# Kernel tuning notes

Hardware: AMD Instinct MI355X
Metric: run time of the kernel (lower is better)

## Reference

```python
import jax, jax.numpy as jnp
import numpy as np

N = 100000      # nodes
E = 1600000     # directed edges (before self loops)
F_IN = 3        # node_feature_dim
H = 32          # hidden_dim
BN_EPS = 1e-5


def _linear_params(k, fan_in, fan_out):
    lim = 1.0 / np.sqrt(fan_in)
    kw, kb = jax.random.split(k)
    W = jax.random.uniform(kw, (fan_in, fan_out), jnp.float32, -lim, lim)
    b = jax.random.uniform(kb, (fan_out,), jnp.float32, -lim, lim)
    return W, b


def setup_inputs() -> dict:
    key = jax.random.key(0)
    ks = jax.random.split(key, 12)
    x = jax.random.normal(ks[0], (N, F_IN), jnp.float32)
    edge_index = jax.random.randint(ks[1], (2, E), 0, N, dtype=jnp.int64)
    node_type = jax.random.randint(ks[2], (N,), 0, 3, dtype=jnp.int64)
    W1, b1 = _linear_params(ks[3], F_IN, H)
    W2, b2 = _linear_params(ks[4], H, H)
    W3, b3 = _linear_params(ks[5], H, H)
    g1 = jnp.ones((H,), jnp.float32); be1 = jnp.zeros((H,), jnp.float32)
    g2 = jnp.ones((H,), jnp.float32); be2 = jnp.zeros((H,), jnp.float32)
    Wc1, bc1 = _linear_params(ks[6], H, H // 2)
    Wc2, bc2 = _linear_params(ks[7], H // 2, 1)
    Wd1, bd1 = _linear_params(ks[8], H, H // 2)
    Wd2, bd2 = _linear_params(ks[9], H // 2, 1)
    return dict(x=x, edge_index=edge_index, node_type=node_type,
                W1=W1, b1=b1, W2=W2, b2=b2, W3=W3, b3=b3,
                g1=g1, be1=be1, g2=g2, be2=be2,
                Wc1=Wc1, bc1=bc1, Wc2=Wc2, bc2=bc2,
                Wd1=Wd1, bd1=bd1, Wd2=Wd2, bd2=bd2)


def reference(x, edge_index, node_type, W1, b1, W2, b2, W3, b3,
              g1, be1, g2, be2, Wc1, bc1, Wc2, bc2, Wd1, bd1, Wd2, bd2):
    n = x.shape[0]
    # GCNConv (PyG default): add self loops, symmetric deg^-1/2 normalization
    loop = jnp.arange(n, dtype=edge_index.dtype)
    src = jnp.concatenate([edge_index[0], loop])  # [E+N]
    dst = jnp.concatenate([edge_index[1], loop])
    deg = jax.ops.segment_sum(jnp.ones_like(dst, dtype=x.dtype), dst, num_segments=n)
    dinv = jnp.where(deg > 0, jax.lax.rsqrt(jnp.maximum(deg, 1.0)), 0.0)
    norm = dinv[src] * dinv[dst]  # [E+N]

    def conv(h, W, b):
        msg = (h @ W)[src] * norm[:, None]                  # gather + scale
        return jax.ops.segment_sum(msg, dst, num_segments=n) + b  # scatter-add

    def bn(h, g, be):  # BatchNorm1d with batch statistics (training math)
        mu = h.mean(axis=0)
        var = ((h - mu) ** 2).mean(axis=0)
        return (h - mu) * jax.lax.rsqrt(var + BN_EPS) * g + be

    h = bn(jax.nn.relu(conv(x, W1, b1)), g1, be1)   # dropout = identity (eval)
    h = bn(jax.nn.relu(conv(h, W2, b2)), g2, be2)
    h = jax.nn.relu(conv(h, W3, b3))

    cand_mask = node_type == 0
    cand_emb = h[cand_mask]                                 # [C, H]
    cand_scores = (jax.nn.relu(cand_emb @ Wc1 + bc1) @ Wc2 + bc2)[:, 0]

    w = jax.nn.softmax(h.sum(axis=1))[:, None]              # [N,1] importance
    g_emb = (h * w).sum(axis=0, keepdims=True)              # [1, H]
    dn = (jax.nn.relu(g_emb @ Wd1 + bd1) @ Wd2 + bd2).reshape(())

    logits = jnp.concatenate([cand_scores, dn[None]], axis=0)
    cand_idx = jnp.nonzero(cand_mask)[0]
    return logits, cand_idx
```

## Files before the change

kernel.cpp:

```cpp
#include <hip/hip_runtime.h>

typedef unsigned int uint;
typedef unsigned char uchar;

#define NB_MAX 256
#define NPB_MAX 2048

#if defined(__has_builtin)
#if __has_builtin(__builtin_amdgcn_cvt_pk_f32_fp8) && __has_builtin(__builtin_amdgcn_cvt_pk_fp8_f32)
#define HW_FP8 1
#endif
#endif

typedef __attribute__((ext_vector_type(2))) float v2f;

static __device__ __forceinline__ uint f2fp8_sw(float v) {
    v = fminf(fmaxf(v, -448.f), 448.f);
    uint u = __float_as_uint(v);
    uint s = (u >> 24) & 0x80u;
    uint mag = u & 0x7FFFFFFFu;
    uint r = mag + 0x7FFFFu + ((mag >> 20) & 1u);
    if (r < 0x3C800000u) return s;
    uint e8 = (r - 0x3C000000u) >> 20;
    return s | min(e8, 0x7Eu);
}
static __device__ __forceinline__ float fp82f(uint b) {
    uint mag = b & 0x7Fu;
    uint bits = ((b & 0x80u) << 24) | ((mag << 20) + 0x3C000000u);
    return mag ? __uint_as_float(bits) : 0.f;
}
static __device__ __forceinline__ void dec8(uint2 v, float* o) {
#ifdef HW_FP8
    v2f a = __builtin_amdgcn_cvt_pk_f32_fp8((int)v.x, false);
    v2f b = __builtin_amdgcn_cvt_pk_f32_fp8((int)v.x, true);
    v2f c = __builtin_amdgcn_cvt_pk_f32_fp8((int)v.y, false);
    v2f d = __builtin_amdgcn_cvt_pk_f32_fp8((int)v.y, true);
    o[0]=a.x; o[1]=a.y; o[2]=b.x; o[3]=b.y;
    o[4]=c.x; o[5]=c.y; o[6]=d.x; o[7]=d.y;
#else
// ... 29 lines not shown
}

static __device__ __forceinline__ unsigned wave_incl_scan(unsigned v) {
    int lane = threadIdx.x & 63;
    #pragma unroll
    for (int d = 1; d < 64; d <<= 1) {
        unsigned t = (unsigned)__shfl_up((int)v, d, 64);
        if (lane >= d) v += t;
    }
    return v;
}

static __device__ void block_excl_scan(const uint* in, uint* out, int n, uint* wscr) {
    int tid = threadIdx.x;
    int lane = tid & 63, wid = tid >> 6;
    int base = tid * 8;
    uint v[8], pre[8], s = 0;
    #pragma unroll
    for (int k = 0; k < 8; k++) v[k] = (base + k < n) ? in[base + k] : 0u;
    #pragma unroll
    for (int k = 0; k < 8; k++) { pre[k] = s; s += v[k]; }
    uint is = wave_incl_scan(s);
    __syncthreads();
    if (lane == 63) wscr[wid] = is;
    __syncthreads();
    uint woff = 0;
    for (int wI = 0; wI < wid; wI++) woff += wscr[wI];
    uint excl = is - s + woff;
    #pragma unroll
    for (int k = 0; k < 8; k++) if (base + k < n) out[base + k] = excl + pre[k];
    __syncthreads();
}

__global__ __launch_bounds__(256) void bucket_hist_kernel(const int* src, const int* dst,
                                                          const int* nt, uint* bcnt, uint* bcand,
                                                          int E, int N, int NB, int shift) {
    __shared__ uint bh[NB_MAX], ch[NB_MAX];
    int tid = threadIdx.x;
    bh[tid] = 0; ch[tid] = 0;
    __syncthreads();
    int gs = gridDim.x * 256;
    for (int i = blockIdx.x * 256 + tid; i < E; i += gs) {
        int d = dst[i], s = src[i];
        if ((uint)d < (uint)N && (uint)s < (uint)N) atomicAdd(&bh[d >> shift], 1u);
    }
    for (int i = blockIdx.x * 256 + tid; i < N; i += gs) {
        if (nt[i] == 0) atomicAdd(&ch[i >> shift], 1u);
    }
    __syncthreads();
    if (bh[tid]) atomicAdd(&bcnt[tid], bh[tid]);
    if (ch[tid]) atomicAdd(&bcand[tid], ch[tid]);
}

__global__ __launch_bounds__(256) void partition_kernel(const int* src, const int* dst,
                                                        const uint* bcnt, uint* alloc0,
                                                        uint* staging, int E, int N, int shift) {
    __shared__ uint bbase_s[NB_MAX];
    __shared__ uint lh[NB_MAX], gb[NB_MAX];
    __shared__ uint ws4[4];
    int tid = threadIdx.x;
    int lane = tid & 63, wid = tid >> 6;
    uint a = bcnt[tid];
    uint ia = wave_incl_scan(a);
    if (lane == 63) ws4[wid] = ia;
    __syncthreads();
    uint off = 0;
    for (int wI = 0; wI < wid; wI++) off += ws4[wI];
    bbase_s[tid] = ia - a + off;
    lh[tid] = 0;
    __syncthreads();
    int base = blockIdx.x * 2048;
    uint mask = (1u << shift) - 1u;
    int breg[8];
    uint rreg[8], pk8[8];
    #pragma unroll
    for (int k = 0; k < 8; k++) {
        int e = base + k * 256 + tid;
        breg[k] = -1;
        if (e < E) {
            int s = src[e], d = dst[e];
            if ((uint)d < (uint)N && (uint)s < (uint)N) {
                int b = d >> shift;
                pk8[k] = (((uint)d & mask) << 17) | (uint)s;
                breg[k] = b;
                rreg[k] = atomicAdd(&lh[b], 1u);
            }
        }
    }
    __syncthreads();
    gb[tid] = lh[tid] ? (bbase_s[tid] + atomicAdd(&alloc0[tid], lh[tid])) : 0u;
    __syncthreads();
    #pragma unroll
    for (int k = 0; k < 8; k++) {
        if (breg[k] >= 0)
            staging[gb[breg[k]] + rreg[k]] = pk8[k];
    }
}

__global__ __launch_bounds__(256) void local_csr_kernel(const uint* staging, const uint* bcnt,
                                                        const uint* bcand, const int* nt,
                                                        const float* x,
                                                        int* csr_src, uint* csr_off, uint* cand_pos,
                                                        float* dinv, float4* xs,
                                                        int N, int shift, int NB) {
    __shared__ uint deg[NPB_MAX];
    __shared__ uint ofs[NPB_MAX];
    __shared__ uint ws4[4];
    __shared__ uint sb[4];
    int b = blockIdx.x, tid = threadIdx.x;
    int lane = tid & 63, wid = tid >> 6;
    uint a = bcnt[tid];
    uint ia = wave_incl_scan(a);
    if (lane == 63) ws4[wid] = ia;
    __syncthreads();
    uint off = 0;
    for (int wI = 0; wI < wid; wI++) off += ws4[wI];
    if (tid == b) { sb[0] = ia - a + off; sb[1] = ia + off; }
    __syncthreads();
    uint c = bcand[tid];
    uint ic = wave_incl_scan(c);
    if (lane == 63) ws4[wid] = ic;
    __syncthreads();
    uint offc = 0;
    for (int wI = 0; wI < wid; wI++) offc += ws4[wI];
    if (tid == b) sb[2] = ic - c + offc;
    __syncthreads();
    uint ebase = sb[0], eend = sb[1], cb = sb[2];
    int nbase = b << shift;
    int ncount = min(1 << shift, N - nbase);
    for (int i = tid; i < ncount; i += 256) deg[i] = 0;
    __syncthreads();
    for (uint p = ebase + tid; p < eend; p += 256)
        atomicAdd(&deg[staging[p] >> 17], 1u);
    __syncthreads();
    block_excl_scan(deg, ofs, ncount, ws4);
    for (int i = tid; i < ncount; i += 256)
        csr_off[nbase + i] = ebase + ofs[i];
    if (b == NB - 1 && tid == 0) csr_off[N] = eend;
    for (int i = tid; i < ncount; i += 256) {
        int g = nbase + i;
        float di = rsqrtf((float)(deg[i] + 1u));
        dinv[g] = di;
        xs[g] = make_float4(x[3*g] * di, x[3*g+1] * di, x[3*g+2] * di, 0.f);
    }
    __syncthreads();
    for (int i = tid; i < ncount; i += 256) deg[i] = 0;
    __syncthreads();
    for (uint p = ebase + tid; p < eend; p += 256) {
        uint pkv = staging[p];
        uint dl = pkv >> 17;
        uint pos = ebase + ofs[dl] + atomicAdd(&deg[dl], 1u);
        csr_src[pos] = (int)(pkv & 0x1FFFFu);
    }
    __syncthreads();
    for (int i = tid; i < ncount; i += 256) deg[i] = (nt[nbase + i] == 0) ? 1u : 0u;
    __syncthreads();
    block_excl_scan(deg, ofs, ncount, ws4);
    for (int i = tid; i < ncount; i += 256) cand_pos[nbase + i] = cb + ofs[i];
}

__global__ __launch_bounds__(256) void agg1_kernel(const float* xs, const int* csr_src,
                                                   const uint* csr_off, const float* dinv,
                                                   const float* W1, const float* b1, uchar* hb,
                                                   int n, float* stats_sum, float* stats_sq,
                                                   uint* gt) {
    const int tid = threadIdx.x;
    const int wave = tid >> 6;
    const int lane = tid & 63;
    const int c4 = lane & 3;
    const int slot = lane >> 2;
    const int qlead = lane & ~3;
    __shared__ float W1s[96];
    __shared__ uint s_lt, s_chunk;
    if (tid < 96) W1s[tid] = W1[tid];
    float bv[8];
    #pragma unroll
    for (int j = 0; j < 8; j++) bv[j] = b1[c4 * 8 + j];
    float bs[8], bq[8];
    #pragma unroll
    for (int j = 0; j < 8; j++) { bs[j] = 0.f; bq[j] = 0.f; }
    __syncthreads();
    while (true) {
        if (tid == 0) s_chunk = atomicAdd(gt, 1u);
        __syncthreads();
        uint cbase = s_chunk * 128u;
        if (cbase >= (uint)n) break;
        uint avail = min((uint)n - cbase, 128u);
        if (tid == 0) s_lt = 0u;
        __syncthreads();
        while (true) {
            uint li = 0;
            if (c4 == 0) li = atomicAdd(&s_lt, 1u);
            li = (uint)__shfl((int)li, qlead, 64);
            if (li >= avail) break;
            uint node = cbase + li;
            uint s = csr_off[node], e = csr_off[node + 1];
            float acc = xs[(size_t)node * 4 + c4];
            for (uint p = s; p < e; p += 8) {
                uint idx[8];
                float wg[8];
                #pragma unroll
                for (int j = 0; j < 8; j++) {
                    uint q = p + (uint)j;
                    uint qc = min(q, e - 1u);
                    idx[j] = (uint)csr_src[qc];
                    wg[j] = (q < e) ? 1.f : 0.f;
                }
                #pragma unroll
                for (int j = 0; j < 8; j++)
                    acc = fmaf(wg[j], xs[(size_t)idx[j] * 4 + c4], acc);
            }
            float u = dinv[node] * acc;
            float u0 = __shfl(u, qlead, 64);
            float u1 = __shfl(u, qlead + 1, 64);
            float u2 = __shfl(u, qlead + 2, 64);
            float hv[8];
            #pragma unroll
            for (int j = 0; j < 8; j++) {
                int ch = c4 * 8 + j;
                float o = u0 * W1s[ch] + u1 * W1s[32 + ch] + u2 * W1s[64 + ch] + bv[j];
                hv[j] = fmaxf(o, 0.f);
            }
            *(uint2*)(hb + (size_t)node * 32 + c4 * 8) = enc8(hv);
            #pragma unroll
            for (int j = 0; j < 8; j++) { bs[j] += hv[j]; bq[j] += hv[j] * hv[j]; }
        }
        __syncthreads();
    }
    #pragma unroll
    for (int m = 4; m < 64; m <<= 1) {
        #pragma unroll
        for (int j = 0; j < 8; j++) {
            bs[j] += __shfl_xor(bs[j], m, 64);
            bq[j] += __shfl_xor(bq[j], m, 64);
        }
    }
    __shared__ float ssum[4][32], ssq[4][32];
    if (slot == 0) {
        #pragma unroll
        for (int j = 0; j < 8; j++) { ssum[wave][c4 * 8 + j] = bs[j]; ssq[wave][c4 * 8 + j] = bq[j]; }
    }
    __syncthreads();
    if (tid < 32) {
        atomicAdd(&stats_sum[tid], ssum[0][tid] + ssum[1][tid] + ssum[2][tid] + ssum[3][tid]);
        atomicAdd(&stats_sq[tid],  ssq[0][tid] + ssq[1][tid] + ssq[2][tid] + ssq[3][tid]);
    }
}

__global__ __launch_bounds__(256) void gemmf_kernel(const uchar* hb, const float* stats_sum,
                                                    const float* stats_sq, const float* g,
                                                    const float* be, const float* W,
                                                    const float* dinv, uchar* zb, int n,
                                                    float inv_n) {
    __shared__ float Ws[1024];
    __shared__ float cs[32];
    __shared__ float a_s[32], d_s[32];
    int tid = threadIdx.x;
    if (tid < 32) {
        float mu = stats_sum[tid] * inv_n;
        float var = fmaxf(stats_sq[tid] * inv_n - mu * mu, 0.f);
        float a = g[tid] * rsqrtf(var + 1e-5f);
        a_s[tid] = a;
        d_s[tid] = be[tid] - mu * a;
    }
    __syncthreads();
    #pragma unroll
    for (int t = tid; t < 1024; t += 256) Ws[t] = a_s[t >> 5] * W[t];
    if (tid < 32) {
        float c = 0.f;
        for (int k = 0; k < 32; k++) c += d_s[k] * W[k * 32 + tid];
        cs[tid] = c;
    }
    __syncthreads();
    int i = blockIdx.x * 256 + tid;
    if (i >= n) return;
    float hk[32], acc[32];
    dec32(hb + (size_t)i * 32, hk);
    #pragma unroll
    for (int j = 0; j < 32; j++) acc[j] = cs[j];
    #pragma unroll
    for (int k = 0; k < 32; k++) {
        float h0 = hk[k];
        #pragma unroll
        for (int j = 0; j < 32; j++) acc[j] += h0 * Ws[k * 32 + j];
    }
    float di = dinv[i];
    #pragma unroll
    for (int j = 0; j < 32; j++) acc[j] *= di;
    enc32(acc, zb + (size_t)i * 32);
}

template<int MODE>
__global__ __launch_bounds__(256) void agg_kernel(const uchar* zb, const int* csr_src,
                                                  const uint* csr_off, const float* dinv,
                                                  const float* bias, uchar* hb, int n,
                                                  float* stats_sum, float* stats_sq,
                                                  float* rowsum, uint* maxkey, uint* gt) {
    const int tid = threadIdx.x;
    const int wave = tid >> 6;
    const int lane = tid & 63;
    const int c4 = lane & 3;
    const int slot = lane >> 2;
    const int qlead = lane & ~3;
    __shared__ uint s_lt, s_chunk;
    float bv[8];
    #pragma unroll
    for (int j = 0; j < 8; j++) bv[j] = bias[c4 * 8 + j];
    float bs[8], bq[8];
    if (MODE == 0) {
        #pragma unroll
        for (int j = 0; j < 8; j++) { bs[j] = 0.f; bq[j] = 0.f; }
    }
    float lmax = -3.0e38f;
    while (true) {
        if (tid == 0) s_chunk = atomicAdd(gt, 1u);
        __syncthreads();
        uint cbase = s_chunk * 128u;
        if (cbase >= (uint)n) break;
        uint avail = min((uint)n - cbase, 128u);
        if (tid == 0) s_lt = 0u;
        __syncthreads();
        while (true) {
            uint li = 0;
            if (c4 == 0) li = atomicAdd(&s_lt, 1u);
            li = (uint)__shfl((int)li, qlead, 64);
            if (li >= avail) break;
            uint node = cbase + li;
            uint s = csr_off[node], e = csr_off[node + 1];
            float acc[8];
            dec8(*(const uint2*)(zb + (size_t)node * 32 + c4 * 8), acc);
            for (uint p = s; p < e; p += 8) {
                uint idx[8];
                float wg[8];
                #pragma unroll
                for (int j = 0; j < 8; j++) {
                    uint q = p + (uint)j;
                    uint qc = min(q, e - 1u);
                    idx[j] = (uint)csr_src[qc];
                    wg[j] = (q < e) ? 1.f : 0.f;
                }
                #pragma unroll
                for (int j = 0; j < 8; j++) {
                    float t[8];
                    dec8(*(const uint2*)(zb + (size_t)idx[j] * 32 + c4 * 8), t);
                    #pragma unroll
                    for (int cI = 0; cI < 8; cI++) acc[cI] = fmaf(wg[j], t[cI], acc[cI]);
                }
            }
            float di = dinv[node];
            float hv[8];
            #pragma unroll
            for (int j = 0; j < 8; j++) hv[j] = fmaxf(di * acc[j] + bv[j], 0.f);
            *(uint2*)(hb + (size_t)node * 32 + c4 * 8) = enc8(hv);
            if (MODE == 0) {
                #pragma unroll
                for (int j = 0; j < 8; j++) { bs[j] += hv[j]; bq[j] += hv[j] * hv[j]; }
            } else {
                float rs = ((hv[0] + hv[1]) + (hv[2] + hv[3])) + ((hv[4] + hv[5]) + (hv[6] + hv[7]));
                rs += __shfl_xor(rs, 1, 64);
                rs += __shfl_xor(rs, 2, 64);
                if (c4 == 0) { rowsum[node] = rs; lmax = fmaxf(lmax, rs); }
            }
        }
        __syncthreads();
    }
    if (MODE == 0) {
        #pragma unroll
        for (int m = 4; m < 64; m <<= 1) {
            #pragma unroll
            for (int j = 0; j < 8; j++) {
                bs[j] += __shfl_xor(bs[j], m, 64);
                bq[j] += __shfl_xor(bq[j], m, 64);
            }
        }
        __shared__ float ssum[4][32], ssq[4][32];
        if (slot == 0) {
            #pragma unroll
            for (int j = 0; j < 8; j++) { ssum[wave][c4 * 8 + j] = bs[j]; ssq[wave][c4 * 8 + j] = bq[j]; }
        }
        __syncthreads();
        if (tid < 32) {
            atomicAdd(&stats_sum[tid], ssum[0][tid] + ssum[1][tid] + ssum[2][tid] + ssum[3][tid]);
            atomicAdd(&stats_sq[tid],  ssq[0][tid] + ssq[1][tid] + ssq[2][tid] + ssq[3][tid]);
        }
    } else {
        #pragma unroll
        for (int m = 1; m < 64; m <<= 1) lmax = fmaxf(lmax, __shfl_xor(lmax, m, 64));
        __shared__ float lm[4];
        if (lane == 0) lm[wave] = lmax;
        __syncthreads();
        if (tid == 0) {
            float m = fmaxf(fmaxf(lm[0], lm[1]), fmaxf(lm[2], lm[3]));
            uint u = __float_as_uint(m);
            uint key = (u & 0x80000000u) ? ~u : (u | 0x80000000u);
            atomicMax(maxkey, key);
        }
    }
}

__global__ __launch_bounds__(256) void head_kernel(const uchar* hb, const int* nt,
                                                   const uint* pos, const float* Wc1,
                                                   const float* bc1, const float* Wc2,
                                                   const float* bc2, const float* rowsum,
                                                   const uint* maxkey, float* gvec, float* Zp,
                                                   uint* ticket, const float* Wd1,
                                                   const float* bd1, const float* Wd2,
                                                   const float* bd2, float* out, int n, int C) {
    __shared__ float W1s[512], b1s[16], W2s[16];
    __shared__ float ls[256];
    __shared__ float ge[32], tt[16];
    __shared__ int lastflag;
    int tid = threadIdx.x;
    for (int t = tid; t < 512; t += 256) W1s[t] = Wc1[t];
    if (tid < 16) { b1s[tid] = bc1[tid]; W2s[tid] = Wc2[tid]; }
    __syncthreads();
    int i = blockIdx.x * 256 + tid;
    if (i < n && nt[i] == 0) {
        float hv[32];
        dec32(hb + (size_t)i * 32, hv);
        float s = bc2[0];
        #pragma unroll
        for (int j = 0; j < 16; j++) {
            float u = b1s[j];
            #pragma unroll
            for (int k = 0; k < 32; k++) u += hv[k] * W1s[k * 16 + j];
            s += fmaxf(u, 0.f) * W2s[j];
        }
        s = fminf(fmaxf(s, -1000.f), 1000.f);
        uint p = pos[i];
        if (p < (uint)C) {
            out[p] = s;
            out[C + 1 + p] = (float)i;
        }
    }
    uint key = *maxkey;
    float M = 0.f;
    if (key != 0u) M = (key & 0x80000000u) ? __uint_as_float(key ^ 0x80000000u) : __uint_as_float(~key);
    int lane = tid & 31, grp = tid >> 5;
    int stride = gridDim.x * 8;
    float accZ = 0.f, accg = 0.f;
    for (int node = blockIdx.x * 8 + grp; node < n; node += stride) {
        float ew = __expf(rowsum[node] - M);
        accg += fp82f(hb[(size_t)node * 32 + lane]) * ew;
        if (lane == 0) accZ += ew;
    }
    ls[tid] = accg;
    __syncthreads();
    if (tid < 32) {
        float a = 0.f;
        #pragma unroll
        for (int g = 0; g < 8; g++) a += ls[tid + 32 * g];
        atomicAdd(&gvec[tid], a);
    }
    __syncthreads();
    ls[tid] = (lane == 0) ? accZ : 0.f;
    __syncthreads();
    if (tid == 0) {
        float a = 0.f;
        for (int t = 0; t < 256; t += 32) a += ls[t];
        atomicAdd(Zp, a);
        __threadfence();
        uint old = atomicAdd(ticket, 1u);
        lastflag = (old == gridDim.x - 1) ? 1 : 0;
    }
    __syncthreads();
    if (lastflag) {
        __threadfence();
        if (tid < 32) ge[tid] = atomicAdd(&gvec[tid], 0.f);
        if (tid == 0) ls[0] = atomicAdd(Zp, 0.f);
        __syncthreads();
        float Zv = fmaxf(ls[0], 1e-30f);
        if (tid < 32) ge[tid] /= Zv;
        __syncthreads();
        if (tid < 16) {
            float s = bd1[tid];
            for (int k = 0; k < 32; k++) s += ge[k] * Wd1[k * 16 + tid];
            tt[tid] = fmaxf(s, 0.f);
        }
        __syncthreads();
        if (tid == 0) {
            float s = bd2[0];
            for (int j = 0; j < 16; j++) s += tt[j] * Wd2[j];
            out[C] = fminf(fmaxf(s, -1000.f), 1000.f);
        }
    }
}

extern "C" void kernel_launch(void* const* d_in, const int* in_sizes, int n_in,
                              void* d_out, int out_size, void* d_ws, size_t ws_size,
                              hipStream_t stream) {
    const float* x   = (const float*)d_in[0];
    const int*   ei  = (const int*)d_in[1];
    const int*   nt  = (const int*)d_in[2];
    const float* W1  = (const float*)d_in[3];  const float* b1  = (const float*)d_in[4];
    const float* W2  = (const float*)d_in[5];  const float* b2  = (const float*)d_in[6];
    const float* W3  = (const float*)d_in[7];  const float* b3  = (const float*)d_in[8];
    const float* g1  = (const float*)d_in[9];  const float* be1 = (const float*)d_in[10];
    const float* g2  = (const float*)d_in[11]; const float* be2 = (const float*)d_in[12];
    const float* Wc1 = (const float*)d_in[13]; const float* bc1 = (const float*)d_in[14];
    const float* Wc2 = (const float*)d_in[15]; const float* bc2 = (const float*)d_in[16];
    const float* Wd1 = (const float*)d_in[17]; const float* bd1 = (const float*)d_in[18];
    const float* Wd2 = (const float*)d_in[19]; const float* bd2 = (const float*)d_in[20];

    const int N = in_sizes[0] / 3;
    const int E = in_sizes[1] / 2;
    const int C = (out_size - 1) / 2;
    const int* e_src = ei;
    const int* e_dst = ei + E;
    float* out = (float*)d_out;

    int shift = 9;
    while (((N + (1 << shift) - 1) >> shift) > NB_MAX) shift++;
    const int NB = (N + (1 << shift) - 1) >> shift;

    char* w = (char*)d_ws;
    auto alloc = [&](size_t bytes) { void* p = (void*)w; w += (bytes + 255) & ~(size_t)255; return p; };
    float*    stats  = (float*)alloc(256 * 4);
    uint*     bcnt   = (uint*)alloc(NB_MAX * 4);
    uint*     bcand  = (uint*)alloc(NB_MAX * 4);
    uint*     alloc0 = (uint*)alloc(NB_MAX * 4);
    size_t zero_bytes = (size_t)((char*)w - (char*)stats);
    float*    dinv   = (float*)alloc((size_t)N * 4);
    uint*     csr_off= (uint*)alloc((size_t)(N + 1) * 4);
    uint*     cand_pos=(uint*)alloc((size_t)N * 4);
    float*    rowsum = (float*)alloc((size_t)N * 4);
    int*      csr_src= (int*)alloc((size_t)E * 4);
    uint*     staging= (uint*)alloc((size_t)E * 4);
    uchar*    zb     = (uchar*)alloc((size_t)N * 32);
    uchar*    hb     = (uchar*)alloc((size_t)N * 32);
    float4*   xs     = (float4*)zb;

    float* sum1 = stats;       float* sq1 = stats + 32;
    float* sum2 = stats + 64;  float* sq2 = stats + 96;
    float* gvec = stats + 128; float* Zp  = stats + 160;
    uint* maxkey = (uint*)(stats + 161);
    uint* ticket = (uint*)(stats + 162);
    uint* gt1 = (uint*)(stats + 163);
    uint* gt2 = (uint*)(stats + 164);
    uint* gt3 = (uint*)(stats + 165);

    hipMemsetAsync(stats, 0, zero_bytes, stream);

    const int gN   = (N + 255) / 256;
    const int gPar = (E + 2047) / 2048;
    int gAgg = (N + 127) / 128;
    if (gAgg > 512) gAgg = 512;
    const float inv_n = 1.0f / (float)N;

    hipLaunchKernelGGL(bucket_hist_kernel, dim3(784), dim3(256), 0, stream, e_src, e_dst, nt, bcnt, bcand, E, N, NB, shift);
    hipLaunchKernelGGL(partition_kernel, dim3(gPar), dim3(256), 0, stream, e_src, e_dst, bcnt, alloc0, staging, E, N, shift);
    hipLaunchKernelGGL(local_csr_kernel, dim3(NB), dim3(256), 0, stream, staging, bcnt, bcand, nt,
                       x, csr_src, csr_off, cand_pos, dinv, xs, N, shift, NB);

    hipLaunchKernelGGL(agg1_kernel, dim3(gAgg), dim3(256), 0, stream, (const float*)xs, csr_src, csr_off,
                       dinv, W1, b1, hb, N, sum1, sq1, gt1);

    hipLaunchKernelGGL(gemmf_kernel, dim3(gN), dim3(256), 0, stream, hb, sum1, sq1, g1, be1, W2, dinv, zb, N, inv_n);
    hipLaunchKernelGGL((agg_kernel<0>), dim3(gAgg), dim3(256), 0, stream, zb, csr_src, csr_off,
                       dinv, b2, hb, N, sum2, sq2, rowsum, maxkey, gt2);

    hipLaunchKernelGGL(gemmf_kernel, dim3(gN), dim3(256), 0, stream, hb, sum2, sq2, g2, be2, W3, dinv, zb, N, inv_n);
    hipLaunchKernelGGL((agg_kernel<1>), dim3(gAgg), dim3(256), 0, stream, zb, csr_src, csr_off,
                       dinv, b3, hb, N, sum1, sq1, rowsum, maxkey, gt3);

    hipLaunchKernelGGL(head_kernel, dim3(gN), dim3(256), 0, stream, hb, nt, cand_pos,
                       Wc1, bc1, Wc2, bc2, rowsum, maxkey, gvec, Zp, ticket,
                       Wd1, bd1, Wd2, bd2, out, N, C);
}
```

Before: 318.1 us.

## Fuse all stages into one persistent kernel with software grid barriers

Replaces the nine separate kernel launches with a single persistent mega-kernel of fixed grid size. Each former kernel becomes a device phase with grid-stride loops, and the phases are separated by atomic-counter grid barriers. Shared memory is merged through a union. This aims to remove launch gaps and per-kernel tail drain. It relies on all 448 blocks being co-resident, otherwise the barriers deadlock, and the fixed grid may underfill or overfill phases that previously had their own grid sizes.

```diff
diff --git a/kernel.cpp b/kernel.cpp
--- a/kernel.cpp
+++ b/kernel.cpp
@@ -5,6 +5,7 @@
 
 #define NB_MAX 256
 #define NPB_MAX 2048
+#define GRID_BLKS 448
 
 #if defined(__has_builtin)
 #if __has_builtin(__builtin_amdgcn_cvt_pk_f32_fp8) && __has_builtin(__builtin_amdgcn_cvt_pk_fp8_f32)
@@ -100,185 +101,211 @@
     __syncthreads();
 }
 
-__global__ __launch_bounds__(256) void bucket_hist_kernel(const int* src, const int* dst,
-                                                          const int* nt, uint* bcnt, uint* bcand,
-                                                          int E, int N, int NB, int shift) {
-    __shared__ uint bh[NB_MAX], ch[NB_MAX];
+union ShU {
+    struct { uint bh[NB_MAX]; uint ch[NB_MAX]; } hist;
+    struct { uint bbase[NB_MAX]; uint lh[NB_MAX]; uint gb[NB_MAX]; uint ws4[4]; } part;
+    struct { uint deg[NPB_MAX]; uint ofs[NPB_MAX]; uint ws4[4]; uint sb[4]; } csr;
+    struct { float Ws[1024]; float cs[32]; float a_s[32]; float d_s[32]; } gemm;
+    struct { float W1s[96]; float ssum[4][32]; float ssq[4][32]; float lm[4]; uint s_lt; uint s_chunk; } agg;
+    struct { float W1s[512]; float b1s[16]; float W2s[16]; float ls[256]; float ge[32]; float tt[16]; } head;
+};
+
+struct MegaP {
+    const float* x;
+    const int* e_src; const int* e_dst; const int* nt;
+    const float *W1,*b1,*W2,*b2,*W3,*b3;
+    const float *g1,*be1,*g2,*be2;
+    const float *Wc1,*bc1,*Wc2,*bc2,*Wd1,*bd1,*Wd2,*bd2;
+    float* stats;
+    uint *bcnt,*bcand,*alloc0;
+    float* dinv; uint* csr_off; uint* cand_pos; float* rowsum;
+    int* csr_src; uint* staging;
+    uchar *zb,*hb;
+    float* out;
+    int N,E,C,NB,shift,nPar;
+    float inv_n;
+};
+
+static __device__ __forceinline__ void gbar(uint* ctr, uint nblk) {
+    __syncthreads();
+    if (threadIdx.x == 0) {
+        __threadfence();
+        uint v = atomicAdd(ctr, 1u) + 1u;
+        while (v < nblk) {
+            __builtin_amdgcn_s_sleep(8);
+            v = __hip_atomic_load(ctr, __ATOMIC_RELAXED, __HIP_MEMORY_SCOPE_AGENT);
+        }
+        __threadfence();
+    }
+    __syncthreads();
+}
+
+static __device__ __forceinline__ void ph_hist(const MegaP& p, ShU& sh) {
     int tid = threadIdx.x;
-    bh[tid] = 0; ch[tid] = 0;
+    sh.hist.bh[tid] = 0; sh.hist.ch[tid] = 0;
     __syncthreads();
     int gs = gridDim.x * 256;
-    for (int i = blockIdx.x * 256 + tid; i < E; i += gs) {
-        int d = dst[i], s = src[i];
-        if ((uint)d < (uint)N && (uint)s < (uint)N) atomicAdd(&bh[d >> shift], 1u);
-    }
-    for (int i = blockIdx.x * 256 + tid; i < N; i += gs) {
-        if (nt[i] == 0) atomicAdd(&ch[i >> shift], 1u);
-    }
-    __syncthreads();
-    if (bh[tid]) atomicAdd(&bcnt[tid], bh[tid]);
-    if (ch[tid]) atomicAdd(&bcand[tid], ch[tid]);
-}
-
-__global__ __launch_bounds__(256) void partition_kernel(const int* src, const int* dst,
-                                                        const uint* bcnt, uint* alloc0,
-                                                        uint* staging, int E, int N, int shift) {
-    __shared__ uint bbase_s[NB_MAX];
-    __shared__ uint lh[NB_MAX], gb[NB_MAX];
-    __shared__ uint ws4[4];
+    for (int i = blockIdx.x * 256 + tid; i < p.E; i += gs) {
+        int d = p.e_dst[i], s = p.e_src[i];
+        if ((uint)d < (uint)p.N && (uint)s < (uint)p.N) atomicAdd(&sh.hist.bh[d >> p.shift], 1u);
+    }
+    for (int i = blockIdx.x * 256 + tid; i < p.N; i += gs) {
+        if (p.nt[i] == 0) atomicAdd(&sh.hist.ch[i >> p.shift], 1u);
+    }
+    __syncthreads();
+    if (sh.hist.bh[tid]) atomicAdd(&p.bcnt[tid], sh.hist.bh[tid]);
+    if (sh.hist.ch[tid]) atomicAdd(&p.bcand[tid], sh.hist.ch[tid]);
+}
+
+static __device__ __forceinline__ void ph_partition(const MegaP& p, ShU& sh) {
     int tid = threadIdx.x;
     int lane = tid & 63, wid = tid >> 6;
-    uint a = bcnt[tid];
+    uint a = p.bcnt[tid];
     uint ia = wave_incl_scan(a);
-    if (lane == 63) ws4[wid] = ia;
+    if (lane == 63) sh.part.ws4[wid] = ia;
     __syncthreads();
     uint off = 0;
-    for (int wI = 0; wI < wid; wI++) off += ws4[wI];
-    bbase_s[tid] = ia - a + off;
-    lh[tid] = 0;
-    __syncthreads();
-    int base = blockIdx.x * 2048;
-    uint mask = (1u << shift) - 1u;
-    int breg[8];
-    uint rreg[8], pk8[8];
-    #pragma unroll
-    for (int k = 0; k < 8; k++) {
-        int e = base + k * 256 + tid;
-        breg[k] = -1;
-        if (e < E) {
-            int s = src[e], d = dst[e];
-            if ((uint)d < (uint)N && (uint)s < (uint)N) {
-                int b = d >> shift;
-                pk8[k] = (((uint)d & mask) << 17) | (uint)s;
-                breg[k] = b;
-                rreg[k] = atomicAdd(&lh[b], 1u);
-            }
-        }
-    }
-    __syncthreads();
-    gb[tid] = lh[tid] ? (bbase_s[tid] + atomicAdd(&alloc0[tid], lh[tid])) : 0u;
-    __syncthreads();
-    #pragma unroll
-    for (int k = 0; k < 8; k++) {
-        if (breg[k] >= 0)
-            staging[gb[breg[k]] + rreg[k]] = pk8[k];
-    }
-}
-
-__global__ __launch_bounds__(256) void local_csr_kernel(const uint* staging, const uint* bcnt,
-                                                        const uint* bcand, const int* nt,
-                                                        const float* x,
-                                                        int* csr_src, uint* csr_off, uint* cand_pos,
-                                                        float* dinv, float4* xs,
-                                                        int N, int shift, int NB) {
-    __shared__ uint deg[NPB_MAX];
-    __shared__ uint ofs[NPB_MAX];
-    __shared__ uint ws4[4];
-    __shared__ uint sb[4];
-    int b = blockIdx.x, tid = threadIdx.x;
+    for (int wI = 0; wI < wid; wI++) off += sh.part.ws4[wI];
+    sh.part.bbase[tid] = ia - a + off;
+    __syncthreads();
+    uint mask = (1u << p.shift) - 1u;
+    for (int cb = blockIdx.x; cb < p.nPar; cb += gridDim.x) {
+        sh.part.lh[tid] = 0;
+        __syncthreads();
+        int base = cb * 2048;
+        int breg[8];
+        uint rreg[8], pk8[8];
+        #pragma unroll
+        for (int k = 0; k < 8; k++) {
+            int e = base + k * 256 + tid;
+            breg[k] = -1;
+            if (e < p.E) {
+                int s = p.e_src[e], d = p.e_dst[e];
+                if ((uint)d < (uint)p.N && (uint)s < (uint)p.N) {
+                    int b = d >> p.shift;
+                    pk8[k] = (((uint)d & mask) << 17) | (uint)s;
+                    breg[k] = b;
+                    rreg[k] = atomicAdd(&sh.part.lh[b], 1u);
+                }
+            }
+        }
+        __syncthreads();
+        sh.part.gb[tid] = sh.part.lh[tid] ? (sh.part.bbase[tid] + atomicAdd(&p.alloc0[tid], sh.part.lh[tid])) : 0u;
+        __syncthreads();
+        #pragma unroll
+        for (int k = 0; k < 8; k++) {
+            if (breg[k] >= 0)
+                p.staging[sh.part.gb[breg[k]] + rreg[k]] = pk8[k];
+        }
+        __syncthreads();
+    }
+}
+
+static __device__ __forceinline__ void ph_localcsr(const MegaP& p, ShU& sh) {
+    int tid = threadIdx.x;
     int lane = tid & 63, wid = tid >> 6;
-    uint a = bcnt[tid];
-    uint ia = wave_incl_scan(a);
-    if (lane == 63) ws4[wid] = ia;
-    __syncthreads();
-    uint off = 0;
-    for (int wI = 0; wI < wid; wI++) off += ws4[wI];
-    if (tid == b) { sb[0] = ia - a + off; sb[1] = ia + off; }
-    __syncthreads();
-    uint c = bcand[tid];
-    uint ic = wave_incl_scan(c);
-    if (lane == 63) ws4[wid] = ic;
-    __syncthreads();
-    uint offc = 0;
-    for (int wI = 0; wI < wid; wI++) offc += ws4[wI];
-    if (tid == b) sb[2] = ic - c + offc;
-    __syncthreads();
-    uint ebase = sb[0], eend = sb[1], cb = sb[2];
-    int nbase = b << shift;
-    int ncount = min(1 << shift, N - nbase);
-    for (int i = tid; i < ncount; i += 256) deg[i] = 0;
-    __syncthreads();
-    for (uint p = ebase + tid; p < eend; p += 256)
-        atomicAdd(&deg[staging[p] >> 17], 1u);
-    __syncthreads();
-    block_excl_scan(deg, ofs, ncount, ws4);
-    for (int i = tid; i < ncount; i += 256)
-        csr_off[nbase + i] = ebase + ofs[i];
-    if (b == NB - 1 && tid == 0) csr_off[N] = eend;
-    for (int i = tid; i < ncount; i += 256) {
-        int g = nbase + i;
-        float di = rsqrtf((float)(deg[i] + 1u));
-        dinv[g] = di;
-        xs[g] = make_float4(x[3*g] * di, x[3*g+1] * di, x[3*g+2] * di, 0.f);
-    }
-    __syncthreads();
-    for (int i = tid; i < ncount; i += 256) deg[i] = 0;
-    __syncthreads();
-    for (uint p = ebase + tid; p < eend; p += 256) {
-        uint pkv = staging[p];
-        uint dl = pkv >> 17;
-        uint pos = ebase + ofs[dl] + atomicAdd(&deg[dl], 1u);
-        csr_src[pos] = (int)(pkv & 0x1FFFFu);
-    }
-    __syncthreads();
-    for (int i = tid; i < ncount; i += 256) deg[i] = (nt[nbase + i] == 0) ? 1u : 0u;
-    __syncthreads();
-    block_excl_scan(deg, ofs, ncount, ws4);
-    for (int i = tid; i < ncount; i += 256) cand_pos[nbase + i] = cb + ofs[i];
-}
-
-__global__ __launch_bounds__(256) void agg1_kernel(const float* xs, const int* csr_src,
-                                                   const uint* csr_off, const float* dinv,
-                                                   const float* W1, const float* b1, uchar* hb,
-                                                   int n, float* stats_sum, float* stats_sq,
-                                                   uint* gt) {
+    float4* xs = (float4*)p.zb;
+    for (int b = blockIdx.x; b < p.NB; b += gridDim.x) {
+        uint a = p.bcnt[tid];
+        uint ia = wave_incl_scan(a);
+        if (lane == 63) sh.csr.ws4[wid] = ia;
+        __syncthreads();
+        uint off = 0;
+        for (int wI = 0; wI < wid; wI++) off += sh.csr.ws4[wI];
+        if (tid == b) { sh.csr.sb[0] = ia - a + off; sh.csr.sb[1] = ia + off; }
+        __syncthreads();
+        uint c = p.bcand[tid];
+        uint ic = wave_incl_scan(c);
+        if (lane == 63) sh.csr.ws4[wid] = ic;
+        __syncthreads();
+        uint offc = 0;
+        for (int wI = 0; wI < wid; wI++) offc += sh.csr.ws4[wI];
+        if (tid == b) sh.csr.sb[2] = ic - c + offc;
+        __syncthreads();
+        uint ebase = sh.csr.sb[0], eend = sh.csr.sb[1], cbv = sh.csr.sb[2];
+        int nbase = b << p.shift;
+        int ncount = min(1 << p.shift, p.N - nbase);
+        for (int i = tid; i < ncount; i += 256) sh.csr.deg[i] = 0;
+        __syncthreads();
+        for (uint q = ebase + tid; q < eend; q += 256)
+            atomicAdd(&sh.csr.deg[p.staging[q] >> 17], 1u);
+        __syncthreads();
+        block_excl_scan(sh.csr.deg, sh.csr.ofs, ncount, sh.csr.ws4);
+        for (int i = tid; i < ncount; i += 256)
+            p.csr_off[nbase + i] = ebase + sh.csr.ofs[i];
+        if (b == p.NB - 1 && tid == 0) p.csr_off[p.N] = eend;
+        for (int i = tid; i < ncount; i += 256) {
+            int g = nbase + i;
+            float di = rsqrtf((float)(sh.csr.deg[i] + 1u));
+            p.dinv[g] = di;
+            xs[g] = make_float4(p.x[3*g] * di, p.x[3*g+1] * di, p.x[3*g+2] * di, 0.f);
+        }
+        __syncthreads();
+        for (int i = tid; i < ncount; i += 256) sh.csr.deg[i] = 0;
+        __syncthreads();
+        for (uint q = ebase + tid; q < eend; q += 256) {
+            uint pkv = p.staging[q];
+            uint dl = pkv >> 17;
+            uint pos = ebase + sh.csr.ofs[dl] + atomicAdd(&sh.csr.deg[dl], 1u);
+            p.csr_src[pos] = (int)(pkv & 0x1FFFFu);
+        }
+        __syncthreads();
+        for (int i = tid; i < ncount; i += 256) sh.csr.deg[i] = (p.nt[nbase + i] == 0) ? 1u : 0u;
+        __syncthreads();
+        block_excl_scan(sh.csr.deg, sh.csr.ofs, ncount, sh.csr.ws4);
+        for (int i = tid; i < ncount; i += 256) p.cand_pos[nbase + i] = cbv + sh.csr.ofs[i];
+        __syncthreads();
+    }
+}
+
+static __device__ __forceinline__ void ph_agg1(const MegaP& p, ShU& sh,
+                                               float* stats_sum, float* stats_sq, uint* gt) {
     const int tid = threadIdx.x;
     const int wave = tid >> 6;
     const int lane = tid & 63;
     const int c4 = lane & 3;
     const int slot = lane >> 2;
     const int qlead = lane & ~3;
-    __shared__ float W1s[96];
-    __shared__ uint s_lt, s_chunk;
-    if (tid < 96) W1s[tid] = W1[tid];
+    const float* xs = (const float*)p.zb;
+    if (tid < 96) sh.agg.W1s[tid] = p.W1[tid];
     float bv[8];
     #pragma unroll
-    for (int j = 0; j < 8; j++) bv[j] = b1[c4 * 8 + j];
+    for (int j = 0; j < 8; j++) bv[j] = p.b1[c4 * 8 + j];
     float bs[8], bq[8];
     #pragma unroll
     for (int j = 0; j < 8; j++) { bs[j] = 0.f; bq[j] = 0.f; }
     __syncthreads();
     while (true) {
-        if (tid == 0) s_chunk = atomicAdd(gt, 1u);
-        __syncthreads();
-        uint cbase = s_chunk * 128u;
-        if (cbase >= (uint)n) break;
-        uint avail = min((uint)n - cbase, 128u);
-        if (tid == 0) s_lt = 0u;
+        if (tid == 0) sh.agg.s_chunk = atomicAdd(gt, 1u);
+        __syncthreads();
+        uint cbase = sh.agg.s_chunk * 128u;
+        if (cbase >= (uint)p.N) break;
+        uint avail = min((uint)p.N - cbase, 128u);
+        if (tid == 0) sh.agg.s_lt = 0u;
         __syncthreads();
         while (true) {
             uint li = 0;
-            if (c4 == 0) li = atomicAdd(&s_lt, 1u);
+            if (c4 == 0) li = atomicAdd(&sh.agg.s_lt, 1u);
             li = (uint)__shfl((int)li, qlead, 64);
             if (li >= avail) break;
             uint node = cbase + li;
-            uint s = csr_off[node], e = csr_off[node + 1];
+            uint s = p.csr_off[node], e = p.csr_off[node + 1];
             float acc = xs[(size_t)node * 4 + c4];
-            for (uint p = s; p < e; p += 8) {
+            for (uint q = s; q < e; q += 8) {
                 uint idx[8];
                 float wg[8];
                 #pragma unroll
                 for (int j = 0; j < 8; j++) {
-                    uint q = p + (uint)j;
-                    uint qc = min(q, e - 1u);
-                    idx[j] = (uint)csr_src[qc];
-                    wg[j] = (q < e) ? 1.f : 0.f;
+                    uint qq = q + (uint)j;
+                    uint qc = min(qq, e - 1u);
+                    idx[j] = (uint)p.csr_src[qc];
+                    wg[j] = (qq < e) ? 1.f : 0.f;
                 }
                 #pragma unroll
                 for (int j = 0; j < 8; j++)
                     acc = fmaf(wg[j], xs[(size_t)idx[j] * 4 + c4], acc);
             }
-            float u = dinv[node] * acc;
+            float u = p.dinv[node] * acc;
             float u0 = __shfl(u, qlead, 64);
             float u1 = __shfl(u, qlead + 1, 64);
             float u2 = __shfl(u, qlead + 2, 64);
@@ -286,10 +313,10 @@
             #pragma unroll
             for (int j = 0; j < 8; j++) {
                 int ch = c4 * 8 + j;
-                float o = u0 * W1s[ch] + u1 * W1s[32 + ch] + u2 * W1s[64 + ch] + bv[j];
+                float o = u0 * sh.agg.W1s[ch] + u1 * sh.agg.W1s[32 + ch] + u2 * sh.agg.W1s[64 + ch] + bv[j];
                 hv[j] = fmaxf(o, 0.f);
             }
-            *(uint2*)(hb + (size_t)node * 32 + c4 * 8) = enc8(hv);
+            *(uint2*)(p.hb + (size_t)node * 32 + c4 * 8) = enc8(hv);
             #pragma unroll
             for (int j = 0; j < 8; j++) { bs[j] += hv[j]; bq[j] += hv[j] * hv[j]; }
         }
@@ -303,74 +330,67 @@
             bq[j] += __shfl_xor(bq[j], m, 64);
         }
     }
-    __shared__ float ssum[4][32], ssq[4][32];
     if (slot == 0) {
         #pragma unroll
-        for (int j = 0; j < 8; j++) { ssum[wave][c4 * 8 + j] = bs[j]; ssq[wave][c4 * 8 + j] = bq[j]; }
+        for (int j = 0; j < 8; j++) { sh.agg.ssum[wave][c4 * 8 + j] = bs[j]; sh.agg.ssq[wave][c4 * 8 + j] = bq[j]; }
     }
     __syncthreads();
     if (tid < 32) {
-        atomicAdd(&stats_sum[tid], ssum[0][tid] + ssum[1][tid] + ssum[2][tid] + ssum[3][tid]);
-        atomicAdd(&stats_sq[tid],  ssq[0][tid] + ssq[1][tid] + ssq[2][tid] + ssq[3][tid]);
-    }
-}
-
-__global__ __launch_bounds__(256) void gemmf_kernel(const uchar* hb, const float* stats_sum,
-                                                    const float* stats_sq, const float* g,
-                                                    const float* be, const float* W,
-                                                    const float* dinv, uchar* zb, int n,
-                                                    float inv_n) {
-    __shared__ float Ws[1024];
-    __shared__ float cs[32];
-    __shared__ float a_s[32], d_s[32];
+        atomicAdd(&stats_sum[tid], sh.agg.ssum[0][tid] + sh.agg.ssum[1][tid] + sh.agg.ssum[2][tid] + sh.agg.ssum[3][tid]);
+        atomicAdd(&stats_sq[tid],  sh.agg.ssq[0][tid] + sh.agg.ssq[1][tid] + sh.agg.ssq[2][tid] + sh.agg.ssq[3][tid]);
+    }
+}
+
+static __device__ __forceinline__ void ph_gemm(const MegaP& p, ShU& sh, const uchar* hb,
+                                               const float* stats_sum, const float* stats_sq,
+                                               const float* g, const float* be, const float* W,
+                                               uchar* zb) {
     int tid = threadIdx.x;
     if (tid < 32) {
-        float mu = stats_sum[tid] * inv_n;
-        float var = fmaxf(stats_sq[tid] * inv_n - mu * mu, 0.f);
+        float mu = stats_sum[tid] * p.inv_n;
+        float var = fmaxf(stats_sq[tid] * p.inv_n - mu * mu, 0.f);
         float a = g[tid] * rsqrtf(var + 1e-5f);
-        a_s[tid] = a;
-        d_s[tid] = be[tid] - mu * a;
-    }
-    __syncthreads();
-    #pragma unroll
-    for (int t = tid; t < 1024; t += 256) Ws[t] = a_s[t >> 5] * W[t];
+        sh.gemm.a_s[tid] = a;
+        sh.gemm.d_s[tid] = be[tid] - mu * a;
+    }
+    __syncthreads();
+    #pragma unroll
+    for (int t = tid; t < 1024; t += 256) sh.gemm.Ws[t] = sh.gemm.a_s[t >> 5] * W[t];
     if (tid < 32) {
         float c = 0.f;
-        for (int k = 0; k < 32; k++) c += d_s[k] * W[k * 32 + tid];
-        cs[tid] = c;
-    }
-    __syncthreads();
-    int i = blockIdx.x * 256 + tid;
-    if (i >= n) return;
-    float hk[32], acc[32];
-    dec32(hb + (size_t)i * 32, hk);
-    #pragma unroll
-    for (int j = 0; j < 32; j++) acc[j] = cs[j];
-    #pragma unroll
-    for (int k = 0; k < 32; k++) {
-        float h0 = hk[k];
-        #pragma unroll
-        for (int j = 0; j < 32; j++) acc[j] += h0 * Ws[k * 32 + j];
-    }
-    float di = dinv[i];
-    #pragma unroll
-    for (int j = 0; j < 32; j++) acc[j] *= di;
-    enc32(acc, zb + (size_t)i * 32);
+        for (int k = 0; k < 32; k++) c += sh.gemm.d_s[k] * W[k * 32 + tid];
+        sh.gemm.cs[tid] = c;
+    }
+    __syncthreads();
+    for (int i = blockIdx.x * 256 + tid; i < p.N; i += gridDim.x * 256) {
+        float hk[32], acc[32];
+        dec32(hb + (size_t)i * 32, hk);
+        #pragma unroll
+        for (int j = 0; j < 32; j++) acc[j] = sh.gemm.cs[j];
+        #pragma unroll
+        for (int k = 0; k < 32; k++) {
+            float h0 = hk[k];
+            #pragma unroll
+            for (int j = 0; j < 32; j++) acc[j] += h0 * sh.gemm.Ws[k * 32 + j];
+        }
+        float di = p.dinv[i];
+        #pragma unroll
+        for (int j = 0; j < 32; j++) acc[j] *= di;
+        enc32(acc, zb + (size_t)i * 32);
+    }
 }
 
 template<int MODE>
-__global__ __launch_bounds__(256) void agg_kernel(const uchar* zb, const int* csr_src,
-                                                  const uint* csr_off, const float* dinv,
-                                                  const float* bias, uchar* hb, int n,
-                                                  float* stats_sum, float* stats_sq,
-                                                  float* rowsum, uint* maxkey, uint* gt) {
+static __device__ __forceinline__ void ph_agg(const MegaP& p, ShU& sh, const uchar* zb,
+                                              const float* bias, uchar* hb,
+                                              float* stats_sum, float* stats_sq,
+                                              float* rowsum, uint* maxkey, uint* gt) {
     const int tid = threadIdx.x;
     const int wave = tid >> 6;
     const int lane = tid & 63;
     const int c4 = lane & 3;
     const int slot = lane >> 2;
     const int qlead = lane & ~3;
-    __shared__ uint s_lt, s_chunk;
     float bv[8];
     #pragma unroll
     for (int j = 0; j < 8; j++) bv[j] = bias[c4 * 8 + j];
@@ -381,31 +401,31 @@
     }
     float lmax = -3.0e38f;
     while (true) {
-        if (tid == 0) s_chunk = atomicAdd(gt, 1u);
-        __syncthreads();
-        uint cbase = s_chunk * 128u;
-        if (cbase >= (uint)n) break;
-        uint avail = min((uint)n - cbase, 128u);
-        if (tid == 0) s_lt = 0u;
+        if (tid == 0) sh.agg.s_chunk = atomicAdd(gt, 1u);
+        __syncthreads();
+        uint cbase = sh.agg.s_chunk * 128u;
+        if (cbase >= (uint)p.N) break;
+        uint avail = min((uint)p.N - cbase, 128u);
+        if (tid == 0) sh.agg.s_lt = 0u;
         __syncthreads();
         while (true) {
             uint li = 0;
-            if (c4 == 0) li = atomicAdd(&s_lt, 1u);
+            if (c4 == 0) li = atomicAdd(&sh.agg.s_lt, 1u);
             li = (uint)__shfl((int)li, qlead, 64);
             if (li >= avail) break;
             uint node = cbase + li;
-            uint s = csr_off[node], e = csr_off[node + 1];
+            uint s = p.csr_off[node], e = p.csr_off[node + 1];
             float acc[8];
             dec8(*(const uint2*)(zb + (size_t)node * 32 + c4 * 8), acc);
-            for (uint p = s; p < e; p += 8) {
+            for (uint q = s; q < e; q += 8) {
                 uint idx[8];
                 float wg[8];
                 #pragma unroll
                 for (int j = 0; j < 8; j++) {
-                    uint q = p + (uint)j;
-                    uint qc = min(q, e - 1u);
-                    idx[j] = (uint)csr_src[qc];
-                    wg[j] = (q < e) ? 1.f : 0.f;
+                    uint qq = q + (uint)j;
+                    uint qc = min(qq, e - 1u);
+                    idx[j] = (uint)p.csr_src[qc];
+                    wg[j] = (qq < e) ? 1.f : 0.f;
                 }
                 #pragma unroll
                 for (int j = 0; j < 8; j++) {
@@ -415,7 +435,7 @@
                     for (int cI = 0; cI < 8; cI++) acc[cI] = fmaf(wg[j], t[cI], acc[cI]);
                 }
             }
-            float di = dinv[node];
+            float di = p.dinv[node];
             float hv[8];
             #pragma unroll
             for (int j = 0; j < 8; j++) hv[j] = fmaxf(di * acc[j] + bv[j], 0.f);
@@ -441,24 +461,22 @@
                 bq[j] += __shfl_xor(bq[j], m, 64);
             }
         }
-        __shared__ float ssum[4][32], ssq[4][32];
         if (slot == 0) {
             #pragma unroll
-            for (int j = 0; j < 8; j++) { ssum[wave][c4 * 8 + j] = bs[j]; ssq[wave][c4 * 8 + j] = bq[j]; }
+            for (int j = 0; j < 8; j++) { sh.agg.ssum[wave][c4 * 8 + j] = bs[j]; sh.agg.ssq[wave][c4 * 8 + j] = bq[j]; }
         }
         __syncthreads();
         if (tid < 32) {
-            atomicAdd(&stats_sum[tid], ssum[0][tid] + ssum[1][tid] + ssum[2][tid] + ssum[3][tid]);
-            atomicAdd(&stats_sq[tid],  ssq[0][tid] + ssq[1][tid] + ssq[2][tid] + ssq[3][tid]);
+            atomicAdd(&stats_sum[tid], sh.agg.ssum[0][tid] + sh.agg.ssum[1][tid] + sh.agg.ssum[2][tid] + sh.agg.ssum[3][tid]);
+            atomicAdd(&stats_sq[tid],  sh.agg.ssq[0][tid] + sh.agg.ssq[1][tid] + sh.agg.ssq[2][tid] + sh.agg.ssq[3][tid]);
         }
     } else {
         #pragma unroll
         for (int m = 1; m < 64; m <<= 1) lmax = fmaxf(lmax, __shfl_xor(lmax, m, 64));
-        __shared__ float lm[4];
-        if (lane == 0) lm[wave] = lmax;
+        if (lane == 0) sh.agg.lm[wave] = lmax;
         __syncthreads();
         if (tid == 0) {
-            float m = fmaxf(fmaxf(lm[0], lm[1]), fmaxf(lm[2], lm[3]));
+            float m = fmaxf(fmaxf(sh.agg.lm[0], sh.agg.lm[1]), fmaxf(sh.agg.lm[2], sh.agg.lm[3]));
             uint u = __float_as_uint(m);
             uint key = (u & 0x80000000u) ? ~u : (u | 0x80000000u);
             atomicMax(maxkey, key);
@@ -466,39 +484,30 @@
     }
 }
 
-__global__ __launch_bounds__(256) void head_kernel(const uchar* hb, const int* nt,
-                                                   const uint* pos, const float* Wc1,
-                                                   const float* bc1, const float* Wc2,
-                                                   const float* bc2, const float* rowsum,
-                                                   const uint* maxkey, float* gvec, float* Zp,
-                                                   uint* ticket, const float* Wd1,
-                                                   const float* bd1, const float* Wd2,
-                                                   const float* bd2, float* out, int n, int C) {
-    __shared__ float W1s[512], b1s[16], W2s[16];
-    __shared__ float ls[256];
-    __shared__ float ge[32], tt[16];
-    __shared__ int lastflag;
+static __device__ __forceinline__ void ph_headAB(const MegaP& p, ShU& sh,
+                                                 float* gvec, float* Zp, const uint* maxkey) {
     int tid = threadIdx.x;
-    for (int t = tid; t < 512; t += 256) W1s[t] = Wc1[t];
-    if (tid < 16) { b1s[tid] = bc1[tid]; W2s[tid] = Wc2[tid]; }
-    __syncthreads();
-    int i = blockIdx.x * 256 + tid;
-    if (i < n && nt[i] == 0) {
-        float hv[32];
-        dec32(hb + (size_t)i * 32, hv);
-        float s = bc2[0];
-        #pragma unroll
-        for (int j = 0; j < 16; j++) {
-            float u = b1s[j];
+    for (int t = tid; t < 512; t += 256) sh.head.W1s[t] = p.Wc1[t];
+    if (tid < 16) { sh.head.b1s[tid] = p.bc1[tid]; sh.head.W2s[tid] = p.Wc2[tid]; }
+    __syncthreads();
+    for (int i = blockIdx.x * 256 + tid; i < p.N; i += gridDim.x * 256) {
+        if (p.nt[i] == 0) {
+            float hv[32];
+            dec32(p.hb + (size_t)i * 32, hv);
+            float s = p.bc2[0];
             #pragma unroll
-            for (int k = 0; k < 32; k++) u += hv[k] * W1s[k * 16 + j];
-            s += fmaxf(u, 0.f) * W2s[j];
-        }
-        s = fminf(fmaxf(s, -1000.f), 1000.f);
-        uint p = pos[i];
-        if (p < (uint)C) {
-            out[p] = s;
-            out[C + 1 + p] = (float)i;
+            for (int j = 0; j < 16; j++) {
+                float u = sh.head.b1s[j];
+                #pragma unroll
+                for (int k = 0; k < 32; k++) u += hv[k] * sh.head.W1s[k * 16 + j];
+                s += fmaxf(u, 0.f) * sh.head.W2s[j];
+            }
+            s = fminf(fmaxf(s, -1000.f), 1000.f);
+            uint pp = p.cand_pos[i];
+            if (pp < (uint)p.C) {
+                p.out[pp] = s;
+                p.out[p.C + 1 + pp] = (float)i;
+            }
         }
     }
     uint key = *maxkey;
@@ -507,51 +516,72 @@
     int lane = tid & 31, grp = tid >> 5;
     int stride = gridDim.x * 8;
     float accZ = 0.f, accg = 0.f;
-    for (int node = blockIdx.x * 8 + grp; node < n; node += stride) {
-        float ew = __expf(rowsum[node] - M);
-        accg += fp82f(hb[(size_t)node * 32 + lane]) * ew;
+    for (int node = blockIdx.x * 8 + grp; node < p.N; node += stride) {
+        float ew = __expf(p.rowsum[node] - M);
+        accg += fp82f(p.hb[(size_t)node * 32 + lane]) * ew;
         if (lane == 0) accZ += ew;
     }
-    ls[tid] = accg;
+    sh.head.ls[tid] = accg;
     __syncthreads();
     if (tid < 32) {
         float a = 0.f;
         #pragma unroll
-        for (int g = 0; g < 8; g++) a += ls[tid + 32 * g];
+        for (int gI = 0; gI < 8; gI++) a += sh.head.ls[tid + 32 * gI];
         atomicAdd(&gvec[tid], a);
     }
     __syncthreads();
-    ls[tid] = (lane == 0) ? accZ : 0.f;
+    sh.head.ls[tid] = (lane == 0) ? accZ : 0.f;
     __syncthreads();
     if (tid == 0) {
         float a = 0.f;
-        for (int t = 0; t < 256; t += 32) a += ls[t];
+        for (int t = 0; t < 256; t += 32) a += sh.head.ls[t];
         atomicAdd(Zp, a);
-        __threadfence();
-        uint old = atomicAdd(ticket, 1u);
-        lastflag = (old == gridDim.x - 1) ? 1 : 0;
-    }
-    __syncthreads();
-    if (lastflag) {
-        __threadfence();
-        if (tid < 32) ge[tid] = atomicAdd(&gvec[tid], 0.f);
-        if (tid == 0) ls[0] = atomicAdd(Zp, 0.f);
-        __syncthreads();
-        float Zv = fmaxf(ls[0], 1e-30f);
-        if (tid < 32) ge[tid] /= Zv;
-        __syncthreads();
-        if (tid < 16) {
-            float s = bd1[tid];
-            for (int k = 0; k < 32; k++) s += ge[k] * Wd1[k * 16 + tid];
-            tt[tid] = fmaxf(s, 0.f);
-        }
-        __syncthreads();
-        if (tid == 0) {
-            float s = bd2[0];
-            for (int j = 0; j < 16; j++) s += tt[j] * Wd2[j];
-            out[C] = fminf(fmaxf(s, -1000.f), 1000.f);
-        }
-    }
+    }
+}
+
+static __device__ __forceinline__ void ph_headC(const MegaP& p, ShU& sh, float* gvec, float* Zp) {
+    int tid = threadIdx.x;
+    if (tid < 32) sh.head.ge[tid] = gvec[tid];
+    if (tid == 0) sh.head.ls[0] = *Zp;
+    __syncthreads();
+    float Zv = fmaxf(sh.head.ls[0], 1e-30f);
+    if (tid < 32) sh.head.ge[tid] /= Zv;
+    __syncthreads();
+    if (tid < 16) {
+        float s = p.bd1[tid];
+        for (int k = 0; k < 32; k++) s += sh.head.ge[k] * p.Wd1[k * 16 + tid];
+        sh.head.tt[tid] = fmaxf(s, 0.f);
+    }
+    __syncthreads();
+    if (tid == 0) {
+        float s = p.bd2[0];
+        for (int j = 0; j < 16; j++) s += sh.head.tt[j] * p.Wd2[j];
+        p.out[p.C] = fminf(fmaxf(s, -1000.f), 1000.f);
+    }
+}
+
+__global__ __launch_bounds__(256, 2) void mega_kernel(MegaP p) {
+    __shared__ ShU sh;
+    float* sum1 = p.stats;        float* sq1 = p.stats + 32;
+    float* sum2 = p.stats + 64;   float* sq2 = p.stats + 96;
+    float* gvec = p.stats + 128;  float* Zp  = p.stats + 160;
+    uint* maxkey = (uint*)(p.stats + 161);
+    uint* gt1 = (uint*)(p.stats + 163);
+    uint* gt2 = (uint*)(p.stats + 164);
+    uint* gt3 = (uint*)(p.stats + 165);
+    uint* bars = (uint*)(p.stats + 168);
+    const uint G = gridDim.x;
+
+    ph_hist(p, sh);                                          gbar(bars + 0, G);
+    ph_partition(p, sh);                                     gbar(bars + 1, G);
+    ph_localcsr(p, sh);                                      gbar(bars + 2, G);
+    ph_agg1(p, sh, sum1, sq1, gt1);                          gbar(bars + 3, G);
+    ph_gemm(p, sh, p.hb, sum1, sq1, p.g1, p.be1, p.W2, p.zb); gbar(bars + 4, G);
+    ph_agg<0>(p, sh, p.zb, p.b2, p.hb, sum2, sq2, p.rowsum, maxkey, gt2); gbar(bars + 5, G);
+    ph_gemm(p, sh, p.hb, sum2, sq2, p.g2, p.be2, p.W3, p.zb); gbar(bars + 6, G);
+    ph_agg<1>(p, sh, p.zb, p.b3, p.hb, sum1, sq1, p.rowsum, maxkey, gt3); gbar(bars + 7, G);
+    ph_headAB(p, sh, gvec, Zp, maxkey);                      gbar(bars + 8, G);
+    if (blockIdx.x == 0) ph_headC(p, sh, gvec, Zp);
 }
 
 extern "C" void kernel_launch(void* const* d_in, const int* in_sizes, int n_in,
@@ -596,42 +626,22 @@
     uint*     staging= (uint*)alloc((size_t)E * 4);
     uchar*    zb     = (uchar*)alloc((size_t)N * 32);
     uchar*    hb     = (uchar*)alloc((size_t)N * 32);
-    float4*   xs     = (float4*)zb;
-
-    float* sum1 = stats;       float* sq1 = stats + 32;
-    float* sum2 = stats + 64;  float* sq2 = stats + 96;
-    float* gvec = stats + 128; float* Zp  = stats + 160;
-    uint* maxkey = (uint*)(stats + 161);
-    uint* ticket = (uint*)(stats + 162);
-    uint* gt1 = (uint*)(stats + 163);
-    uint* gt2 = (uint*)(stats + 164);
-    uint* gt3 = (uint*)(stats + 165);
 
     hipMemsetAsync(stats, 0, zero_bytes, stream);
 
-    const int gN   = (N + 255) / 256;
-    const int gPar = (E + 2047) / 2048;
-    int gAgg = (N + 127) / 128;
-    if (gAgg > 512) gAgg = 512;
-    const float inv_n = 1.0f / (float)N;
-
-    hipLaunchKernelGGL(bucket_hist_kernel, dim3(784), dim3(256), 0, stream, e_src, e_dst, nt, bcnt, bcand, E, N, NB, shift);
-    hipLaunchKernelGGL(partition_kernel, dim3(gPar), dim3(256), 0, stream, e_src, e_dst, bcnt, alloc0, staging, E, N, shift);
-    hipLaunchKernelGGL(local_csr_kernel, dim3(NB), dim3(256), 0, stream, staging, bcnt, bcand, nt,
-                       x, csr_src, csr_off, cand_pos, dinv, xs, N, shift, NB);
-
-    hipLaunchKernelGGL(agg1_kernel, dim3(gAgg), dim3(256), 0, stream, (const float*)xs, csr_src, csr_off,
-                       dinv, W1, b1, hb, N, sum1, sq1, gt1);
-
-    hipLaunchKernelGGL(gemmf_kernel, dim3(gN), dim3(256), 0, stream, hb, sum1, sq1, g1, be1, W2, dinv, zb, N, inv_n);
-    hipLaunchKernelGGL((agg_kernel<0>), dim3(gAgg), dim3(256), 0, stream, zb, csr_src, csr_off,
-                       dinv, b2, hb, N, sum2, sq2, rowsum, maxkey, gt2);
-
-    hipLaunchKernelGGL(gemmf_kernel, dim3(gN), dim3(256), 0, stream, hb, sum2, sq2, g2, be2, W3, dinv, zb, N, inv_n);
-    hipLaunchKernelGGL((agg_kernel<1>), dim3(gAgg), dim3(256), 0, stream, zb, csr_src, csr_off,
-                       dinv, b3, hb, N, sum1, sq1, rowsum, maxkey, gt3);
-
-    hipLaunchKernelGGL(head_kernel, dim3(gN), dim3(256), 0, stream, hb, nt, cand_pos,
-                       Wc1, bc1, Wc2, bc2, rowsum, maxkey, gvec, Zp, ticket,
-                       Wd1, bd1, Wd2, bd2, out, N, C);
-}
+    MegaP mp;
+    mp.x = x; mp.e_src = e_src; mp.e_dst = e_dst; mp.nt = nt;
+    mp.W1 = W1; mp.b1 = b1; mp.W2 = W2; mp.b2 = b2; mp.W3 = W3; mp.b3 = b3;
+    mp.g1 = g1; mp.be1 = be1; mp.g2 = g2; mp.be2 = be2;
+    mp.Wc1 = Wc1; mp.bc1 = bc1; mp.Wc2 = Wc2; mp.bc2 = bc2;
+    mp.Wd1 = Wd1; mp.bd1 = bd1; mp.Wd2 = Wd2; mp.bd2 = bd2;
+    mp.stats = stats; mp.bcnt = bcnt; mp.bcand = bcand; mp.alloc0 = alloc0;
+    mp.dinv = dinv; mp.csr_off = csr_off; mp.cand_pos = cand_pos; mp.rowsum = rowsum;
+    mp.csr_src = csr_src; mp.staging = staging; mp.zb = zb; mp.hb = hb;
+    mp.out = out;
+    mp.N = N; mp.E = E; mp.C = C; mp.NB = NB; mp.shift = shift;
+    mp.nPar = (E + 2047) / 2048;
+    mp.inv_n = 1.0f / (float)N;
+
+    hipLaunchKernelGGL(mega_kernel, dim3(GRID_BLKS), dim3(256), 0, stream, mp);
+}
```

After: 917.5 us. 2.88x slower.
